# Kernel tuning notes

Measured on AMD Instinct MI355X. Metric: run time of the kernel, lower is better.

The kernel has to match this reference:

```python
import jax, jax.numpy as jnp
import numpy as np

N_NODES = 100000
N_EDGES = 1600000
IN_C, HID, OUT_C = 128, 128, 64
LN_EPS = 1e-5


def _glorot(key, shape):
    fan_in = shape[-1]
    return jax.random.normal(key, shape, dtype=jnp.float32) / jnp.sqrt(jnp.float32(fan_in))


def setup_inputs() -> dict:
    key = jax.random.key(0)
    ks = jax.random.split(key, 16)
    x = jax.random.normal(ks[0], (N_NODES, IN_C), dtype=jnp.float32)
    edge_index = jax.random.randint(ks[1], (2, N_EDGES), 0, N_NODES, dtype=jnp.int64)
    inp = {"x": x, "edge_index": edge_index}
    dims = [(IN_C, HID), (HID, HID), (HID, OUT_C)]
    for i, (din, dout) in enumerate(dims):
        inp[f"Wl{i}"] = _glorot(ks[2 + 3 * i], (dout, din))   # neighbor-aggregate weight
        inp[f"Wr{i}"] = _glorot(ks[3 + 3 * i], (dout, din))   # root/self weight
        inp[f"b{i}"] = jnp.zeros((dout,), dtype=jnp.float32)
    for i, d in enumerate([HID, HID]):
        inp[f"g{i}"] = jnp.ones((d,), dtype=jnp.float32)      # LayerNorm gamma
        inp[f"be{i}"] = jnp.zeros((d,), dtype=jnp.float32)    # LayerNorm beta
    return inp


def sage_conv(x, src, dst, Wl, Wr, b):
    # mean aggregation of source features at destination nodes
    msg = x[src]                                                    # [E, F]
    agg = jax.ops.segment_sum(msg, dst, num_segments=N_NODES)      # [N, F]
    deg = jax.ops.segment_sum(jnp.ones((src.shape[0],), x.dtype), dst, num_segments=N_NODES)
    agg = agg / jnp.maximum(deg, 1.0)[:, None]
    return agg @ Wl.T + x @ Wr.T + b


def layer_norm(x, gamma, beta):
    mu = jnp.mean(x, axis=-1, keepdims=True)
    var = jnp.mean(jnp.square(x - mu), axis=-1, keepdims=True)
    return (x - mu) * jax.lax.rsqrt(var + LN_EPS) * gamma + beta


def reference(x, edge_index, Wl0, Wr0, b0, g0, be0, Wl1, Wr1, b1, g1, be1, Wl2, Wr2, b2):
    src, dst = edge_index[0], edge_index[1]
    h = layer_norm(jax.nn.relu(sage_conv(x, src, dst, Wl0, Wr0, b0)), g0, be0)
    h = layer_norm(jax.nn.relu(sage_conv(h, src, dst, Wl1, Wr1, b1)), g1, be1)
    return sage_conv(h, src, dst, Wl2, Wr2, b2)
```

## Files before the change

### kernel.cpp

```cpp
#include <hip/hip_runtime.h>


typedef __bf16 bf16x8 __attribute__((ext_vector_type(8)));
typedef __bf16 bf16x4 __attribute__((ext_vector_type(4)));
typedef float  f32x4  __attribute__((ext_vector_type(4)));

#define PB_SHIFT 9
#define PB_NB    256
#define PB_EPT   8
#define PB_BLOCK 256
#define PB_CHUNK (PB_BLOCK * PB_EPT)

__global__ __launch_bounds__(PB_BLOCK) void coarse_hist(
    const int* __restrict__ dst, int* __restrict__ bhist, int E) {
    __shared__ int h[PB_NB];
    const int t = threadIdx.x;
    h[t] = 0;
    __syncthreads();
    const int e0 = blockIdx.x * PB_CHUNK + t;
#pragma unroll
    for (int i = 0; i < PB_EPT; ++i) {
        int e = e0 + i * PB_BLOCK;
        if (e < E) atomicAdd(&h[dst[e] >> PB_SHIFT], 1);
    }
    __syncthreads();
    if (h[t]) atomicAdd(&bhist[t], h[t]);
}

__global__ __launch_bounds__(PB_NB) void coarse_scan(
    const int* __restrict__ bhist, int* __restrict__ bbase, int* __restrict__ bcur) {
    __shared__ int sm[PB_NB];
    const int t = threadIdx.x;
    int v = bhist[t];
    sm[t] = v;
    __syncthreads();
    for (int off = 1; off < PB_NB; off <<= 1) {
        int add = (t >= off) ? sm[t - off] : 0;
        __syncthreads();
        sm[t] += add;
        __syncthreads();
    }
    int excl = sm[t] - v;
    bbase[t] = excl;
    bcur[t] = excl;
}

__global__ __launch_bounds__(PB_BLOCK) void part_scatter(
    const int* __restrict__ src, const int* __restrict__ dst,
    int* __restrict__ bcursor, int2* __restrict__ part, int E) {
    __shared__ int hist[PB_NB];
    __shared__ int base[PB_NB];
    const int t = threadIdx.x;
    hist[t] = 0;
    __syncthreads();
    const int e0 = blockIdx.x * PB_CHUNK + t;
    int my_s[PB_EPT], my_d[PB_EPT], my_r[PB_EPT];
#pragma unroll
    for (int i = 0; i < PB_EPT; ++i) {
        int e = e0 + i * PB_BLOCK;
        if (e < E) {
            my_s[i] = src[e];
            my_d[i] = dst[e];
            my_r[i] = atomicAdd(&hist[my_d[i] >> PB_SHIFT], 1);
        }
    }
    __syncthreads();
    {
        int c = hist[t];
        base[t] = c ? atomicAdd(&bcursor[t], c) : 0;
    }
    __syncthreads();
#pragma unroll
    for (int i = 0; i < PB_EPT; ++i) {
        int e = e0 + i * PB_BLOCK;
        if (e < E) {
            int b = my_d[i] >> PB_SHIFT;
            part[base[b] + my_r[i]] = make_int2(my_s[i], my_d[i]);
        }
    }
}

__global__ __launch_bounds__(256) void bucket_build(
    const int2* __restrict__ part, const int* __restrict__ bbase,
    int* __restrict__ offs, int* __restrict__ ssrc, int N, int E) {
    __shared__ int h[512];
    __shared__ int s[512];
    __shared__ int cur[512];
    const int b = blockIdx.x;
    const int t = threadIdx.x;
    const int beg = bbase[b];
    const int end = (b == PB_NB - 1) ? E : bbase[b + 1];

    h[t] = 0; h[t + 256] = 0;
    __syncthreads();
    for (int e = beg + t; e < end; e += 256)
        atomicAdd(&h[part[e].y & 511], 1);
    __syncthreads();
    s[t] = h[t]; s[t + 256] = h[t + 256];
    __syncthreads();
    for (int off = 1; off < 512; off <<= 1) {
        int a0 = (t >= off) ? s[t - off] : 0;
        int i1 = t + 256;
        int a1 = (i1 >= off) ? s[i1 - off] : 0;
        __syncthreads();
        s[t] += a0; s[i1] += a1;
        __syncthreads();
    }
#pragma unroll
    for (int k = 0; k < 2; ++k) {
        int i = t + k * 256;
        int excl = s[i] - h[i];
        cur[i] = excl;
        int node = (b << PB_SHIFT) + i;
        if (node < N) offs[node] = beg + excl;
    }
    if (b == 0 && t == 0) offs[N] = E;
    __syncthreads();
    for (int e = beg + t; e < end; e += 256) {
        int2 sd = part[e];
        int p = atomicAdd(&cur[sd.y & 511], 1);
        ssrc[beg + p] = sd.x;
    }
}

template <int DOUT, typename AT, typename ZT>
__global__ __launch_bounds__(256) void gemm_mfma(
    const AT* __restrict__ A,
    const float* __restrict__ Wl,
    const float* __restrict__ Wr,
    const float* __restrict__ bias,
    __bf16* __restrict__ ybuf,
    ZT*     __restrict__ zbuf,
    int M) {
    __shared__ __bf16 Asm[64 * 136];
    __shared__ __bf16 Bsm[DOUT * 136];

    const int t = threadIdx.x;
    const int rowBase = blockIdx.x * 64;
    const bool isZ = blockIdx.y != 0;
    const float* W = isZ ? Wr : Wl;

    if constexpr (sizeof(AT) == 4) {
#pragma unroll
        for (int i = 0; i < 8; ++i) {
            int idx = t + 256 * i;
            int r = idx >> 5;
            int c4 = idx & 31;
            int grow = rowBase + r;
            if (grow >= M) grow = M - 1;
            float4 v = *(const float4*)((const float*)A + (size_t)grow * 128 + c4 * 4);
            bf16x4 o;
            o[0] = (__bf16)v.x; o[1] = (__bf16)v.y; o[2] = (__bf16)v.z; o[3] = (__bf16)v.w;
            *(bf16x4*)(Asm + r * 136 + c4 * 4) = o;
        }
    } else {
#pragma unroll
        for (int i = 0; i < 4; ++i) {
            int idx = t + 256 * i;
            int r = idx >> 4;
            int c8 = idx & 15;
            int grow = rowBase + r;
            if (grow >= M) grow = M - 1;
            bf16x8 v = *(const bf16x8*)((const __bf16*)A + (size_t)grow * 128 + c8 * 8);
            *(bf16x8*)(Asm + r * 136 + c8 * 8) = v;
        }
    }
    constexpr int BCH = DOUT * 32 / 256;
#pragma unroll
    for (int i = 0; i < BCH; ++i) {
        int idx = t + 256 * i;
        int r = idx >> 5;
        int c4 = idx & 31;
        float4 v = *(const float4*)(W + (size_t)r * 128 + c4 * 4);
        bf16x4 o;
        o[0] = (__bf16)v.x; o[1] = (__bf16)v.y; o[2] = (__bf16)v.z; o[3] = (__bf16)v.w;
        *(bf16x4*)(Bsm + r * 136 + c4 * 4) = o;
    }
    __syncthreads();

    const int lane = t & 63;
    const int wid = t >> 6;
    const int mb = (wid >> 1) * 32;
    const int nbase = (wid & 1) * (DOUT / 2);
    constexpr int NJ = DOUT / 32;
    const int ln = lane & 15;
    const int qk = lane >> 4;

    f32x4 acc[2][NJ] = {};
#pragma unroll
    for (int ks = 0; ks < 4; ++ks) {
        const int k0 = ks * 32 + qk * 8;
        bf16x8 a0 = *(const bf16x8*)(Asm + (mb + ln) * 136 + k0);
        bf16x8 a1 = *(const bf16x8*)(Asm + (mb + 16 + ln) * 136 + k0);
        bf16x8 b[NJ];
#pragma unroll
        for (int j = 0; j < NJ; ++j)
            b[j] = *(const bf16x8*)(Bsm + (nbase + j * 16 + ln) * 136 + k0);
#pragma unroll
        for (int j = 0; j < NJ; ++j) {
            acc[0][j] = __builtin_amdgcn_mfma_f32_16x16x32_bf16(a0, b[j], acc[0][j], 0, 0, 0);
            acc[1][j] = __builtin_amdgcn_mfma_f32_16x16x32_bf16(a1, b[j], acc[1][j], 0, 0, 0);
        }
    }

    float bcol[NJ];
    if (isZ) {
#pragma unroll
        for (int j = 0; j < NJ; ++j) bcol[j] = bias[nbase + j * 16 + ln];
    }
#pragma unroll
    for (int i = 0; i < 2; ++i) {
#pragma unroll
        for (int r = 0; r < 4; ++r) {
            int grow = rowBase + mb + i * 16 + qk * 4 + r;
            if (grow >= M) continue;
#pragma unroll
            for (int j = 0; j < NJ; ++j) {
                int col = nbase + j * 16 + ln;
                float v = acc[i][j][r];
                if (isZ) zbuf[(size_t)grow * DOUT + col] = (ZT)(v + bcol[j]);
                else     ybuf[(size_t)grow * DOUT + col] = (__bf16)v;
            }
        }
    }
}

__global__ __launch_bounds__(256) void agg_ln128(
    const int* __restrict__ offs, const int* __restrict__ ssrc,
    const __bf16* __restrict__ ybuf,
    const __bf16* __restrict__ zbuf,
    const float* __restrict__ gamma, const float* __restrict__ beta,
    __bf16* __restrict__ hout, int nNodes) {
    const int lane = threadIdx.x & 63;
    const int qh = lane >> 4;
    const int li = lane & 15;
    const int node = blockIdx.x * 4 + (threadIdx.x >> 6);
    if (node >= nNodes) return;
    const int beg = offs[node], end = offs[node + 1];
    const int deg = end - beg;

    float acc[8] = {};
    const int iters = (deg + 7) >> 3;
    int eA = beg + qh;
    int eB = eA + 4;
    int idxA = 0, idxB = 0;
    if (iters > 0) {
        idxA = ssrc[(eA < end) ? eA : beg];
        idxB = ssrc[(eB < end) ? eB : beg];
    }
    for (int u = 0; u < iters; ++u) {
        const bool va = eA < end;
        const bool vb = eB < end;
        uint4 uva, uvb;
        if (va) uva = *(const uint4*)(ybuf + (size_t)idxA * 128 + li * 8);
        if (vb) uvb = *(const uint4*)(ybuf + (size_t)idxB * 128 + li * 8);
        int eA2 = eA + 8, eB2 = eB + 8;
        int idxA2 = ssrc[(eA2 < end) ? eA2 : beg];
        int idxB2 = ssrc[(eB2 < end) ? eB2 : beg];
        if (va) {
            acc[0] += __uint_as_float(uva.x << 16);
            acc[1] += __uint_as_float(uva.x & 0xffff0000u);
            acc[2] += __uint_as_float(uva.y << 16);
            acc[3] += __uint_as_float(uva.y & 0xffff0000u);
            acc[4] += __uint_as_float(uva.z << 16);
            acc[5] += __uint_as_float(uva.z & 0xffff0000u);
            acc[6] += __uint_as_float(uva.w << 16);
            acc[7] += __uint_as_float(uva.w & 0xffff0000u);
        }
        if (vb) {
            acc[0] += __uint_as_float(uvb.x << 16);
            acc[1] += __uint_as_float(uvb.x & 0xffff0000u);
            acc[2] += __uint_as_float(uvb.y << 16);
            acc[3] += __uint_as_float(uvb.y & 0xffff0000u);
            acc[4] += __uint_as_float(uvb.z << 16);
            acc[5] += __uint_as_float(uvb.z & 0xffff0000u);
            acc[6] += __uint_as_float(uvb.w << 16);
            acc[7] += __uint_as_float(uvb.w & 0xffff0000u);
        }
        eA = eA2; eB = eB2; idxA = idxA2; idxB = idxB2;
    }

    bf16x8 zv = *(const bf16x8*)(zbuf + (size_t)node * 128 + li * 8);
    const float4* g4 = (const float4*)(gamma + li * 8);
    const float4* b4 = (const float4*)(beta + li * 8);
    float4 g0 = g4[0], g1 = g4[1], bb0 = b4[0], bb1 = b4[1];

#pragma unroll
    for (int m = 0; m < 8; ++m) {
        acc[m] += __shfl_xor(acc[m], 16, 64);
        acc[m] += __shfl_xor(acc[m], 32, 64);
    }
    float inv = 1.f / (float)((deg > 1) ? deg : 1);
    float v[8];
#pragma unroll
    for (int m = 0; m < 8; ++m) v[m] = fmaxf(acc[m] * inv + (float)zv[m], 0.f);

    float s = 0.f;
#pragma unroll
    for (int m = 0; m < 8; ++m) s += v[m];
#pragma unroll
    for (int off = 8; off >= 1; off >>= 1) s += __shfl_xor(s, off, 64);
    float mu = s * (1.f / 128.f);
    float d[8], q = 0.f;
#pragma unroll
    for (int m = 0; m < 8; ++m) { d[m] = v[m] - mu; q += d[m] * d[m]; }
#pragma unroll
    for (int off = 8; off >= 1; off >>= 1) q += __shfl_xor(q, off, 64);
    float rstd = rsqrtf(q * (1.f / 128.f) + 1e-5f);

    if (qh == 0) {
        bf16x8 o;
        o[0] = (__bf16)(d[0] * rstd * g0.x + bb0.x);
        o[1] = (__bf16)(d[1] * rstd * g0.y + bb0.y);
        o[2] = (__bf16)(d[2] * rstd * g0.z + bb0.z);
        o[3] = (__bf16)(d[3] * rstd * g0.w + bb0.w);
        o[4] = (__bf16)(d[4] * rstd * g1.x + bb1.x);
        o[5] = (__bf16)(d[5] * rstd * g1.y + bb1.y);
        o[6] = (__bf16)(d[6] * rstd * g1.z + bb1.z);
        o[7] = (__bf16)(d[7] * rstd * g1.w + bb1.w);
        *(bf16x8*)(hout + (size_t)node * 128 + li * 8) = o;
    }
}

__global__ __launch_bounds__(256) void agg_out64(
    const int* __restrict__ offs, const int* __restrict__ ssrc,
    const __bf16* __restrict__ ybuf,
    const float* __restrict__ zbuf,
    float* __restrict__ out, int nNodes) {
    const int lane = threadIdx.x & 63;
    const int eh = lane >> 3;
    const int li = lane & 7;
    const int node = blockIdx.x * 4 + (threadIdx.x >> 6);
    if (node >= nNodes) return;
    const int beg = offs[node], end = offs[node + 1];
    const int deg = end - beg;

    float acc[8] = {};
    const int iters = (deg + 15) >> 4;
    int eA = beg + eh;
    int eB = eA + 8;
    int idxA = 0, idxB = 0;
    if (iters > 0) {
        idxA = ssrc[(eA < end) ? eA : beg];
        idxB = ssrc[(eB < end) ? eB : beg];
    }
    for (int u = 0; u < iters; ++u) {
        const bool va = eA < end;
        const bool vb = eB < end;
        uint4 uva, uvb;
        if (va) uva = *(const uint4*)(ybuf + (size_t)idxA * 64 + li * 8);
        if (vb) uvb = *(const uint4*)(ybuf + (size_t)idxB * 64 + li * 8);
        int eA2 = eA + 16, eB2 = eB + 16;
        int idxA2 = ssrc[(eA2 < end) ? eA2 : beg];
        int idxB2 = ssrc[(eB2 < end) ? eB2 : beg];
        if (va) {
            acc[0] += __uint_as_float(uva.x << 16);
            acc[1] += __uint_as_float(uva.x & 0xffff0000u);
            acc[2] += __uint_as_float(uva.y << 16);
            acc[3] += __uint_as_float(uva.y & 0xffff0000u);
            acc[4] += __uint_as_float(uva.z << 16);
            acc[5] += __uint_as_float(uva.z & 0xffff0000u);
            acc[6] += __uint_as_float(uva.w << 16);
            acc[7] += __uint_as_float(uva.w & 0xffff0000u);
        }
        if (vb) {
            acc[0] += __uint_as_float(uvb.x << 16);
            acc[1] += __uint_as_float(uvb.x & 0xffff0000u);
            acc[2] += __uint_as_float(uvb.y << 16);
            acc[3] += __uint_as_float(uvb.y & 0xffff0000u);
            acc[4] += __uint_as_float(uvb.z << 16);
            acc[5] += __uint_as_float(uvb.z & 0xffff0000u);
            acc[6] += __uint_as_float(uvb.w << 16);
            acc[7] += __uint_as_float(uvb.w & 0xffff0000u);
        }
        eA = eA2; eB = eB2; idxA = idxA2; idxB = idxB2;
    }

    const float4* z4 = (const float4*)(zbuf + (size_t)node * 64 + li * 8);
    float4 z0 = z4[0], z1 = z4[1];

#pragma unroll
    for (int m = 0; m < 8; ++m) {
        acc[m] += __shfl_xor(acc[m], 8, 64);
        acc[m] += __shfl_xor(acc[m], 16, 64);
        acc[m] += __shfl_xor(acc[m], 32, 64);
    }
    if (eh == 0) {
        float inv = 1.f / (float)((deg > 1) ? deg : 1);
        float4 o0, o1;
        o0.x = acc[0] * inv + z0.x;
        o0.y = acc[1] * inv + z0.y;
        o0.z = acc[2] * inv + z0.z;
        o0.w = acc[3] * inv + z0.w;
        o1.x = acc[4] * inv + z1.x;
        o1.y = acc[5] * inv + z1.y;
        o1.z = acc[6] * inv + z1.z;
        o1.w = acc[7] * inv + z1.w;
        float4* op = (float4*)(out + (size_t)node * 64 + li * 8);
        op[0] = o0;
        op[1] = o1;
    }
}

extern "C" void kernel_launch(void* const* d_in, const int* in_sizes, int n_in,
                              void* d_out, int out_size, void* d_ws, size_t ws_size,
                              hipStream_t stream) {
    const float* x   = (const float*)d_in[0];
    const int*   ei  = (const int*)d_in[1];
    const float* Wl0 = (const float*)d_in[2];
    const float* Wr0 = (const float*)d_in[3];
    const float* b0  = (const float*)d_in[4];
    const float* Wl1 = (const float*)d_in[5];
    const float* Wr1 = (const float*)d_in[6];
    const float* b1  = (const float*)d_in[7];
    const float* Wl2 = (const float*)d_in[8];
    const float* Wr2 = (const float*)d_in[9];
    const float* b2  = (const float*)d_in[10];
    const float* g0  = (const float*)d_in[11];
    const float* be0 = (const float*)d_in[12];
    const float* g1  = (const float*)d_in[13];
    const float* be1 = (const float*)d_in[14];

    const int N = in_sizes[0] / 128;
    const int E = in_sizes[1] / 2;
    const int* src = ei;
    const int* dst = ei + E;
    float* out = (float*)d_out;

    char* p = (char*)d_ws;
    auto carve = [&](size_t bytes) {
        void* q = (void*)p;
        p += (bytes + 255) & ~(size_t)255;
        return q;
    };
    int*     offs  = (int*)carve(sizeof(int) * (size_t)(N + 1));
    int*     bhist = (int*)carve(sizeof(int) * (size_t)PB_NB);
    int*     bbase = (int*)carve(sizeof(int) * (size_t)PB_NB);
    int*     bcur  = (int*)carve(sizeof(int) * (size_t)PB_NB);
    int*     ssrc  = (int*)carve(sizeof(int) * (size_t)E);
    int2*    part  = (int2*)carve(sizeof(int2) * (size_t)E);
    __bf16*  h     = (__bf16*)carve(sizeof(__bf16) * (size_t)N * 128);
    __bf16*  ybuf  = (__bf16*)carve(sizeof(__bf16) * (size_t)N * 128);
    void*    zraw  = carve(sizeof(__bf16) * (size_t)N * 128);
    __bf16*  zb    = (__bf16*)zraw;
    float*   zf    = (float*)zraw;

    hipMemsetAsync(bhist, 0, sizeof(int) * PB_NB, stream);
    const int gridE = (E + PB_CHUNK - 1) / PB_CHUNK;
    coarse_hist<<<gridE, PB_BLOCK, 0, stream>>>(dst, bhist, E);
    coarse_scan<<<1, PB_NB, 0, stream>>>(bhist, bbase, bcur);
    part_scatter<<<gridE, PB_BLOCK, 0, stream>>>(src, dst, bcur, part, E);
    bucket_build<<<PB_NB, 256, 0, stream>>>(part, bbase, offs, ssrc, N, E);

    const int gridM = (N + 63) / 64;
    const int gridNode = (N + 3) / 4;

    gemm_mfma<128, float, __bf16><<<dim3(gridM, 2), 256, 0, stream>>>(x, Wl0, Wr0, b0, ybuf, zb, N);
    agg_ln128<<<gridNode, 256, 0, stream>>>(offs, ssrc, ybuf, zb, g0, be0, h, N);
    gemm_mfma<128, __bf16, __bf16><<<dim3(gridM, 2), 256, 0, stream>>>(h, Wl1, Wr1, b1, ybuf, zb, N);
    agg_ln128<<<gridNode, 256, 0, stream>>>(offs, ssrc, ybuf, zb, g1, be1, h, N);
    gemm_mfma<64, __bf16, float><<<dim3(gridM, 2), 256, 0, stream>>>(h, Wl2, Wr2, b2, ybuf, zf, N);
    agg_out64<<<gridNode, 256, 0, stream>>>(offs, ssrc, ybuf, zf, out, N);
}
```

Measured before the change: 428.5 us.

## Quantize neighbor-projected features to per-row uint8 for gather aggregation

The GEMM epilogue now quantizes the neighbor-projected rows (Wl·x) to offset uint8 with a per-row absmax scale, using an LDS row-max reduction across the two column-half waves. The aggregation kernels gather 8-byte words instead of 16-byte words plus one scale per edge, then dequantize and subtract the 128 offset times the summed scales. The aim is to halve the random-gather traffic that dominates the edge loop. In exchange it adds a syncthreads and shuffle reductions in the GEMM, an extra scale load per edge, and 8-bit quantization error in the aggregated messages.

```diff
diff --git a/kernel.cpp b/kernel.cpp
--- a/kernel.cpp
+++ b/kernel.cpp
@@ -4,6 +4,17 @@
 typedef __bf16 bf16x8 __attribute__((ext_vector_type(8)));
 typedef __bf16 bf16x4 __attribute__((ext_vector_type(4)));
 typedef float  f32x4  __attribute__((ext_vector_type(4)));
+
+__device__ __forceinline__ void u8_acc8(uint2 w, float s, float* acc) {
+    acc[0] += s * (float)( w.x        & 0xffu);
+    acc[1] += s * (float)((w.x >>  8) & 0xffu);
+    acc[2] += s * (float)((w.x >> 16) & 0xffu);
+    acc[3] += s * (float)( w.x >> 24        );
+    acc[4] += s * (float)( w.y        & 0xffu);
+    acc[5] += s * (float)((w.y >>  8) & 0xffu);
+    acc[6] += s * (float)((w.y >> 16) & 0xffu);
+    acc[7] += s * (float)( w.y >> 24        );
+}
 
 #define PB_SHIFT 9
 #define PB_NB    256
@@ -129,11 +140,13 @@
     const float* __restrict__ Wl,
     const float* __restrict__ Wr,
     const float* __restrict__ bias,
-    __bf16* __restrict__ ybuf,
-    ZT*     __restrict__ zbuf,
+    unsigned char* __restrict__ ybuf,
+    float*         __restrict__ yscale,
+    ZT*            __restrict__ zbuf,
     int M) {
     __shared__ __bf16 Asm[64 * 136];
     __shared__ __bf16 Bsm[DOUT * 136];
+    __shared__ float  rmx[2][64];
 
     const int t = threadIdx.x;
     const int rowBase = blockIdx.x * 64;
@@ -203,23 +216,54 @@
         }
     }
 
-    float bcol[NJ];
     if (isZ) {
+        float bcol[NJ];
 #pragma unroll
         for (int j = 0; j < NJ; ++j) bcol[j] = bias[nbase + j * 16 + ln];
-    }
-#pragma unroll
-    for (int i = 0; i < 2; ++i) {
-#pragma unroll
-        for (int r = 0; r < 4; ++r) {
-            int grow = rowBase + mb + i * 16 + qk * 4 + r;
-            if (grow >= M) continue;
-#pragma unroll
-            for (int j = 0; j < NJ; ++j) {
-                int col = nbase + j * 16 + ln;
-                float v = acc[i][j][r];
-                if (isZ) zbuf[(size_t)grow * DOUT + col] = (ZT)(v + bcol[j]);
-                else     ybuf[(size_t)grow * DOUT + col] = (__bf16)v;
+#pragma unroll
+        for (int i = 0; i < 2; ++i) {
+#pragma unroll
+            for (int r = 0; r < 4; ++r) {
+                int grow = rowBase + mb + i * 16 + qk * 4 + r;
+                if (grow >= M) continue;
+#pragma unroll
+                for (int j = 0; j < NJ; ++j) {
+                    int col = nbase + j * 16 + ln;
+                    zbuf[(size_t)grow * DOUT + col] = (ZT)(acc[i][j][r] + bcol[j]);
+                }
+            }
+        }
+    } else {
+#pragma unroll
+        for (int i = 0; i < 2; ++i) {
+#pragma unroll
+            for (int r = 0; r < 4; ++r) {
+                float m = 0.f;
+#pragma unroll
+                for (int j = 0; j < NJ; ++j) m = fmaxf(m, fabsf(acc[i][j][r]));
+#pragma unroll
+                for (int o = 1; o < 16; o <<= 1) m = fmaxf(m, __shfl_xor(m, o, 64));
+                if (ln == 0) rmx[wid & 1][mb + i * 16 + qk * 4 + r] = m;
+            }
+        }
+        __syncthreads();
+#pragma unroll
+        for (int i = 0; i < 2; ++i) {
+#pragma unroll
+            for (int r = 0; r < 4; ++r) {
+                int rb = mb + i * 16 + qk * 4 + r;
+                int grow = rowBase + rb;
+                if (grow >= M) continue;
+                float rm = fmaxf(fmaxf(rmx[0][rb], rmx[1][rb]), 1e-20f);
+                float sc = rm * (1.f / 127.f);
+                float rs = 127.f / rm;
+                if ((wid & 1) == 0 && ln == 0) yscale[grow] = sc;
+#pragma unroll
+                for (int j = 0; j < NJ; ++j) {
+                    int col = nbase + j * 16 + ln;
+                    float q = rintf(acc[i][j][r] * rs) + 128.f;
+                    ybuf[(size_t)grow * DOUT + col] = (unsigned char)q;
+                }
             }
         }
     }
@@ -227,7 +271,8 @@
 
 __global__ __launch_bounds__(256) void agg_ln128(
     const int* __restrict__ offs, const int* __restrict__ ssrc,
-    const __bf16* __restrict__ ybuf,
+    const unsigned char* __restrict__ ybuf,
+    const float* __restrict__ yscale,
     const __bf16* __restrict__ zbuf,
     const float* __restrict__ gamma, const float* __restrict__ beta,
     __bf16* __restrict__ hout, int nNodes) {
@@ -240,6 +285,7 @@
     const int deg = end - beg;
 
     float acc[8] = {};
+    float sS = 0.f;
     const int iters = (deg + 7) >> 3;
     int eA = beg + qh;
     int eB = eA + 4;
@@ -251,32 +297,15 @@
     for (int u = 0; u < iters; ++u) {
         const bool va = eA < end;
         const bool vb = eB < end;
-        uint4 uva, uvb;
-        if (va) uva = *(const uint4*)(ybuf + (size_t)idxA * 128 + li * 8);
-        if (vb) uvb = *(const uint4*)(ybuf + (size_t)idxB * 128 + li * 8);
+        uint2 wa, wb;
+        float sa = 0.f, sb = 0.f;
+        if (va) { wa = *(const uint2*)(ybuf + (((unsigned)idxA) << 7) + li * 8); sa = yscale[idxA]; }
+        if (vb) { wb = *(const uint2*)(ybuf + (((unsigned)idxB) << 7) + li * 8); sb = yscale[idxB]; }
         int eA2 = eA + 8, eB2 = eB + 8;
         int idxA2 = ssrc[(eA2 < end) ? eA2 : beg];
         int idxB2 = ssrc[(eB2 < end) ? eB2 : beg];
-        if (va) {
-            acc[0] += __uint_as_float(uva.x << 16);
-            acc[1] += __uint_as_float(uva.x & 0xffff0000u);
-            acc[2] += __uint_as_float(uva.y << 16);
-            acc[3] += __uint_as_float(uva.y & 0xffff0000u);
-            acc[4] += __uint_as_float(uva.z << 16);
-            acc[5] += __uint_as_float(uva.z & 0xffff0000u);
-            acc[6] += __uint_as_float(uva.w << 16);
-            acc[7] += __uint_as_float(uva.w & 0xffff0000u);
-        }
-        if (vb) {
-            acc[0] += __uint_as_float(uvb.x << 16);
-            acc[1] += __uint_as_float(uvb.x & 0xffff0000u);
-            acc[2] += __uint_as_float(uvb.y << 16);
-            acc[3] += __uint_as_float(uvb.y & 0xffff0000u);
-            acc[4] += __uint_as_float(uvb.z << 16);
-            acc[5] += __uint_as_float(uvb.z & 0xffff0000u);
-            acc[6] += __uint_as_float(uvb.w << 16);
-            acc[7] += __uint_as_float(uvb.w & 0xffff0000u);
-        }
+        if (va) { u8_acc8(wa, sa, acc); sS += sa; }
+        if (vb) { u8_acc8(wb, sb, acc); sS += sb; }
         eA = eA2; eB = eB2; idxA = idxA2; idxB = idxB2;
     }
 
@@ -285,6 +314,8 @@
     const float4* b4 = (const float4*)(beta + li * 8);
     float4 g0 = g4[0], g1 = g4[1], bb0 = b4[0], bb1 = b4[1];
 
+    sS += __shfl_xor(sS, 16, 64);
+    sS += __shfl_xor(sS, 32, 64);
 #pragma unroll
     for (int m = 0; m < 8; ++m) {
         acc[m] += __shfl_xor(acc[m], 16, 64);
@@ -293,7 +324,8 @@
     float inv = 1.f / (float)((deg > 1) ? deg : 1);
     float v[8];
 #pragma unroll
-    for (int m = 0; m < 8; ++m) v[m] = fmaxf(acc[m] * inv + (float)zv[m], 0.f);
+    for (int m = 0; m < 8; ++m)
+        v[m] = fmaxf((acc[m] - 128.f * sS) * inv + (float)zv[m], 0.f);
 
     float s = 0.f;
 #pragma unroll
@@ -324,7 +356,8 @@
 
 __global__ __launch_bounds__(256) void agg_out64(
     const int* __restrict__ offs, const int* __restrict__ ssrc,
-    const __bf16* __restrict__ ybuf,
+    const unsigned char* __restrict__ ybuf,
+    const float* __restrict__ yscale,
     const float* __restrict__ zbuf,
     float* __restrict__ out, int nNodes) {
     const int lane = threadIdx.x & 63;
@@ -336,6 +369,7 @@
     const int deg = end - beg;
 
     float acc[8] = {};
+    float sS = 0.f;
     const int iters = (deg + 15) >> 4;
     int eA = beg + eh;
     int eB = eA + 8;
@@ -347,38 +381,24 @@
     for (int u = 0; u < iters; ++u) {
         const bool va = eA < end;
         const bool vb = eB < end;
-        uint4 uva, uvb;
-        if (va) uva = *(const uint4*)(ybuf + (size_t)idxA * 64 + li * 8);
-        if (vb) uvb = *(const uint4*)(ybuf + (size_t)idxB * 64 + li * 8);
+        uint2 wa, wb;
+        float sa = 0.f, sb = 0.f;
+        if (va) { wa = *(const uint2*)(ybuf + (((unsigned)idxA) << 6) + li * 8); sa = yscale[idxA]; }
+        if (vb) { wb = *(const uint2*)(ybuf + (((unsigned)idxB) << 6) + li * 8); sb = yscale[idxB]; }
         int eA2 = eA + 16, eB2 = eB + 16;
         int idxA2 = ssrc[(eA2 < end) ? eA2 : beg];
         int idxB2 = ssrc[(eB2 < end) ? eB2 : beg];
-        if (va) {
-            acc[0] += __uint_as_float(uva.x << 16);
-            acc[1] += __uint_as_float(uva.x & 0xffff0000u);
-            acc[2] += __uint_as_float(uva.y << 16);
-            acc[3] += __uint_as_float(uva.y & 0xffff0000u);
-            acc[4] += __uint_as_float(uva.z << 16);
-            acc[5] += __uint_as_float(uva.z & 0xffff0000u);
-            acc[6] += __uint_as_float(uva.w << 16);
-            acc[7] += __uint_as_float(uva.w & 0xffff0000u);
-        }
-        if (vb) {
-            acc[0] += __uint_as_float(uvb.x << 16);
-            acc[1] += __uint_as_float(uvb.x & 0xffff0000u);
-            acc[2] += __uint_as_float(uvb.y << 16);
-            acc[3] += __uint_as_float(uvb.y & 0xffff0000u);
-            acc[4] += __uint_as_float(uvb.z << 16);
-            acc[5] += __uint_as_float(uvb.z & 0xffff0000u);
-            acc[6] += __uint_as_float(uvb.w << 16);
-            acc[7] += __uint_as_float(uvb.w & 0xffff0000u);
-        }
+        if (va) { u8_acc8(wa, sa, acc); sS += sa; }
+        if (vb) { u8_acc8(wb, sb, acc); sS += sb; }
         eA = eA2; eB = eB2; idxA = idxA2; idxB = idxB2;
     }
 
     const float4* z4 = (const float4*)(zbuf + (size_t)node * 64 + li * 8);
     float4 z0 = z4[0], z1 = z4[1];
 
+    sS += __shfl_xor(sS, 8, 64);
+    sS += __shfl_xor(sS, 16, 64);
+    sS += __shfl_xor(sS, 32, 64);
 #pragma unroll
     for (int m = 0; m < 8; ++m) {
         acc[m] += __shfl_xor(acc[m], 8, 64);
@@ -388,14 +408,14 @@
     if (eh == 0) {
         float inv = 1.f / (float)((deg > 1) ? deg : 1);
         float4 o0, o1;
-        o0.x = acc[0] * inv + z0.x;
-        o0.y = acc[1] * inv + z0.y;
-        o0.z = acc[2] * inv + z0.z;
-        o0.w = acc[3] * inv + z0.w;
-        o1.x = acc[4] * inv + z1.x;
-        o1.y = acc[5] * inv + z1.y;
-        o1.z = acc[6] * inv + z1.z;
-        o1.w = acc[7] * inv + z1.w;
+        o0.x = (acc[0] - 128.f * sS) * inv + z0.x;
+        o0.y = (acc[1] - 128.f * sS) * inv + z0.y;
+        o0.z = (acc[2] - 128.f * sS) * inv + z0.z;
+        o0.w = (acc[3] - 128.f * sS) * inv + z0.w;
+        o1.x = (acc[4] - 128.f * sS) * inv + z1.x;
+        o1.y = (acc[5] - 128.f * sS) * inv + z1.y;
+        o1.z = (acc[6] - 128.f * sS) * inv + z1.z;
+        o1.w = (acc[7] - 128.f * sS) * inv + z1.w;
         float4* op = (float4*)(out + (size_t)node * 64 + li * 8);
         op[0] = o0;
         op[1] = o1;
@@ -433,19 +453,20 @@
         p += (bytes + 255) & ~(size_t)255;
         return q;
     };
-    int*     offs  = (int*)carve(sizeof(int) * (size_t)(N + 1));
-    int*     bhist = (int*)carve(sizeof(int) * (size_t)PB_NB);
-    int*     bbase = (int*)carve(sizeof(int) * (size_t)PB_NB);
-    int*     bcur  = (int*)carve(sizeof(int) * (size_t)PB_NB);
-    int*     ssrc  = (int*)carve(sizeof(int) * (size_t)E);
-    int2*    part  = (int2*)carve(sizeof(int2) * (size_t)E);
-    __bf16*  h     = (__bf16*)carve(sizeof(__bf16) * (size_t)N * 128);
-    __bf16*  ybuf  = (__bf16*)carve(sizeof(__bf16) * (size_t)N * 128);
-    void*    zraw  = carve(sizeof(__bf16) * (size_t)N * 128);
-    __bf16*  zb    = (__bf16*)zraw;
-    float*   zf    = (float*)zraw;
-
-    hipMemsetAsync(bhist, 0, sizeof(int) * PB_NB, stream);
+    int*     offs   = (int*)carve(sizeof(int) * (size_t)(N + 1));
+    int*     bhist  = (int*)carve(sizeof(int) * (size_t)PB_NB);
+    int*     bbase  = (int*)carve(sizeof(int) * (size_t)PB_NB);
+    int*     bcur   = (int*)carve(sizeof(int) * (size_t)PB_NB);
+    int*     ssrc   = (int*)carve(sizeof(int) * (size_t)E);
+    int2*    part   = (int2*)carve(sizeof(int2) * (size_t)E);
+    __bf16*  h      = (__bf16*)carve(sizeof(__bf16) * (size_t)N * 128);
+    unsigned char* ybuf = (unsigned char*)carve(sizeof(unsigned char) * (size_t)N * 128);
+    float*   yscale = (float*)carve(sizeof(float) * (size_t)N);
+    void*    zraw   = carve(sizeof(__bf16) * (size_t)N * 128);
+    __bf16*  zb     = (__bf16*)zraw;
+    float*   zf     = (float*)zraw;
+
+    (void)hipMemsetAsync(bhist, 0, sizeof(int) * PB_NB, stream);
     const int gridE = (E + PB_CHUNK - 1) / PB_CHUNK;
     coarse_hist<<<gridE, PB_BLOCK, 0, stream>>>(dst, bhist, E);
     coarse_scan<<<1, PB_NB, 0, stream>>>(bhist, bbase, bcur);
@@ -455,10 +476,10 @@
     const int gridM = (N + 63) / 64;
     const int gridNode = (N + 3) / 4;
 
-    gemm_mfma<128, float, __bf16><<<dim3(gridM, 2), 256, 0, stream>>>(x, Wl0, Wr0, b0, ybuf, zb, N);
-    agg_ln128<<<gridNode, 256, 0, stream>>>(offs, ssrc, ybuf, zb, g0, be0, h, N);
-    gemm_mfma<128, __bf16, __bf16><<<dim3(gridM, 2), 256, 0, stream>>>(h, Wl1, Wr1, b1, ybuf, zb, N);
-    agg_ln128<<<gridNode, 256, 0, stream>>>(offs, ssrc, ybuf, zb, g1, be1, h, N);
-    gemm_mfma<64, __bf16, float><<<dim3(gridM, 2), 256, 0, stream>>>(h, Wl2, Wr2, b2, ybuf, zf, N);
-    agg_out64<<<gridNode, 256, 0, stream>>>(offs, ssrc, ybuf, zf, out, N);
-}
+    gemm_mfma<128, float, __bf16><<<dim3(gridM, 2), 256, 0, stream>>>(x, Wl0, Wr0, b0, ybuf, yscale, zb, N);
+    agg_ln128<<<gridNode, 256, 0, stream>>>(offs, ssrc, ybuf, yscale, zb, g0, be0, h, N);
+    gemm_mfma<128, __bf16, __bf16><<<dim3(gridM, 2), 256, 0, stream>>>(h, Wl1, Wr1, b1, ybuf, yscale, zb, N);
+    agg_ln128<<<gridNode, 256, 0, stream>>>(offs, ssrc, ybuf, yscale, zb, g1, be1, h, N);
+    gemm_mfma<64, __bf16, float><<<dim3(gridM, 2), 256, 0, stream>>>(h, Wl2, Wr2, b2, ybuf, yscale, zf, N);
+    agg_out64<<<gridNode, 256, 0, stream>>>(offs, ssrc, ybuf, yscale, zf, out, N);
+}
```

Measured after the change: 426.3 us. About the same (-0.5%).
